# Performance work log

Measured on AMD Instinct MI355X. Metric: run time of the kernel, lower is better.

The kernel has to match this reference:

```python
import jax, jax.numpy as jnp
import numpy as np

N_VISITS, N_PROC, N_MED = 64, 32, 16
V_DIAG, V_PROC, V_MED = 2000, 1500, 4000
EMB, EMB_FF = 256, 128


def _normalize(adj):
    # row-normalize(adj + I), matching GCN.normalize
    adj = adj + np.eye(adj.shape[0], dtype=np.float32)
    rs = adj.sum(1)
    rinv = np.where(rs > 0, 1.0 / rs, 0.0).astype(np.float32)
    return (adj * rinv[:, None]).astype(np.float32)


def setup_inputs() -> dict:
    key = jax.random.key(0)
    ks = jax.random.split(key, 24)
    rng = np.random.default_rng(0)
    ehr = (rng.random((V_MED, V_MED)) < 0.01).astype(np.float32)
    ddi = (rng.random((V_MED, V_MED)) < 0.01).astype(np.float32)
    s = 0.02
    return {
        'proc_codes': jax.random.randint(ks[0], (N_VISITS, N_PROC), 0, V_DIAG + V_PROC + 2),
        'med_codes': jax.random.randint(ks[1], (N_VISITS, N_MED), 0, V_MED),
        'emb_table': jax.random.normal(ks[2], (V_DIAG + V_PROC + 2, EMB_FF)) * s,
        'conv_w': jax.random.normal(ks[3], (3,)) * 0.3,
        'conv_b': jnp.zeros((1,)),
        'wq': jax.random.normal(ks[4], (EMB_FF, EMB)) * s,
        'wk': jax.random.normal(ks[5], (EMB_FF, EMB)) * s,
        'wv': jax.random.normal(ks[6], (EMB_FF, EMB)) * s,
        'wr': jax.random.normal(ks[7], (EMB, EMB)) * s,
        'alpha': jax.random.normal(ks[8], (EMB,)),
        'beta': jax.random.normal(ks[9], (EMB,)),
        'ehr_adj_norm': jnp.asarray(_normalize(ehr)),
        'ddi_adj_norm': jnp.asarray(_normalize(ddi)),
        'ddi_adj_raw': jnp.asarray(ddi),
        'ehr_w1': jax.random.normal(ks[10], (V_MED, EMB)) * s,
        'ehr_b1': jnp.zeros((EMB,)),
        'ehr_w2': jax.random.normal(ks[11], (EMB, EMB)) * s,
        'ehr_b2': jnp.zeros((EMB,)),
        'ddi_w1': jax.random.normal(ks[12], (V_MED, EMB)) * s,
        'ddi_b1': jnp.zeros((EMB,)),
        'ddi_w2': jax.random.normal(ks[13], (EMB, EMB)) * s,
        'ddi_b2': jnp.zeros((EMB,)),
        'inter': jax.random.normal(ks[14], (1,)) * 0.1,
        'out_w1': jax.random.normal(ks[15], (3 * EMB, 2 * EMB)) * s,
        'out_b1': jnp.zeros((2 * EMB,)),
        'out_w2': jax.random.normal(ks[16], (2 * EMB, V_MED)) * s,
        'out_b2': jnp.zeros((V_MED,)),
    }


def _fastformer(x, wq, wk, wv, wr, alpha, beta):
    # x: (1, n, EMB_FF); additive linear attention (all-ones mask => no-op)
    q = x @ wq  # (1, n, EMB)
    k = x @ wk
    v = x @ wv
    scale = EMB ** -0.5
    aw = jax.nn.softmax(q * alpha * scale, axis=-1)
    gq = jnp.sum(q * aw, axis=1)              # global query (1, EMB)
    p = gq[:, None, :] * k                    # (1, n, EMB)
    bw = jax.nn.softmax(p * beta * scale, axis=-1)
    gk = jnp.sum(p * bw, axis=1)              # global key (1, EMB)
    return (gk[:, None, :] * v) @ wr + q


def _gcn(adj, w1, b1, w2, b2):
    # input x = I, so first layer support is just w1
    h = jax.nn.relu(adj @ w1 + b1)
    return adj @ (h @ w2) + b2


def reference(proc_codes, med_codes, emb_table, conv_w, conv_b, wq, wk, wv, wr, alpha, beta,
              ehr_adj_norm, ddi_adj_norm, ddi_adj_raw,
              ehr_w1, ehr_b1, ehr_w2, ehr_b2, ddi_w1, ddi_b1, ddi_w2, ddi_b2,
              inter, out_w1, out_b1, out_w2, out_b2):
    n = proc_codes.shape[0]
    # per-admission mean embedding  (n, EMB_FF)
    i2 = emb_table[proc_codes].mean(axis=1)
    # Conv1d(1,1,k=3,same) over the feature dim, then ReLU
    xp = jnp.pad(i2, ((0, 0), (1, 1)))
    i2 = jax.nn.relu(conv_w[0] * xp[:, :-2] + conv_w[1] * xp[:, 1:-1] + conv_w[2] * xp[:, 2:] + conv_b)
    feat = _fastformer(i2[None], wq, wk, wv, wr, alpha, beta)[0]  # (n, EMB)
    query = feat[-1:]
    drug_memory = _gcn(ehr_adj_norm, ehr_w1, ehr_b1, ehr_w2, ehr_b2) \
        - _gcn(ddi_adj_norm, ddi_w1, ddi_b1, ddi_w2, ddi_b2) * inter[0]
    key_w1 = jax.nn.softmax(query @ drug_memory.T, axis=-1)   # (1, V_MED)
    fact1 = key_w1 @ drug_memory                              # (1, EMB)
    # history (len(input) > 1): multi-hot med history values
    history_keys = feat[:-1]
    hv = jnp.zeros((n - 1, V_MED), dtype=feat.dtype)
    hv = hv.at[jnp.arange(n - 1)[:, None], med_codes[:-1]].set(1.0)
    visit_w = jax.nn.softmax(query @ history_keys.T, axis=-1)
    fact2 = (visit_w @ hv) @ drug_memory
    h = jnp.concatenate([query, fact1, fact2], axis=-1)       # (1, 3*EMB)
    result = jax.nn.relu(h @ out_w1 + out_b1) @ out_w2 + out_b2
    sp = jax.nn.sigmoid(result)[0]
    batch_neg = 0.0005 * jnp.einsum('i,ij,j->', sp, ddi_adj_raw, sp)
    return result, batch_neg
```

## Files before the change

kernel.cpp:

```cpp
#include <hip/hip_runtime.h>
#include <hip/hip_bf16.h>

#define NV 64
#define NP 32
#define NM 16
#define VMED 4000
#define EMB 256
#define EMBFF 128
#define CAP 128


__device__ __forceinline__ float block_sum_256(float v, float* red) {
    int t = threadIdx.x;
    red[t] = v; __syncthreads();
    for (int s = 128; s > 0; s >>= 1) { if (t < s) red[t] += red[t + s]; __syncthreads(); }
    float r = red[0]; __syncthreads();
    return r;
}
__device__ __forceinline__ float block_max_256(float v, float* red) {
    int t = threadIdx.x;
    red[t] = v; __syncthreads();
    for (int s = 128; s > 0; s >>= 1) { if (t < s) red[t] = fmaxf(red[t], red[t + s]); __syncthreads(); }
    float r = red[0]; __syncthreads();
    return r;
}

__global__ void k_embed_conv(const int* __restrict__ proc, const float* __restrict__ emb,
                             const float* __restrict__ cw, const float* __restrict__ cb,
                             float* __restrict__ i2) {
    __shared__ float sm[EMBFF + 2];
    int v = blockIdx.x, f = threadIdx.x;
    float s = 0.f;
    for (int c = 0; c < NP; c++) s += emb[proc[v * NP + c] * EMBFF + f];
    sm[f + 1] = s * (1.0f / NP);
    if (f == 0) { sm[0] = 0.f; sm[EMBFF + 1] = 0.f; }
    __syncthreads();
    float o = cw[0] * sm[f] + cw[1] * sm[f + 1] + cw[2] * sm[f + 2] + cb[0];
    i2[v * EMBFF + f] = o > 0.f ? o : 0.f;
}

__global__ void k_qkv(const float* __restrict__ i2, const float* __restrict__ wq,
                      const float* __restrict__ wk, const float* __restrict__ wv,
                      const float* __restrict__ alpha,
                      float* __restrict__ q, float* __restrict__ k, float* __restrict__ v,
                      float* __restrict__ qaw) {
    __shared__ float x[EMBFF];
    __shared__ float red[256];
    int vi = blockIdx.x, f = threadIdx.x;
    if (f < EMBFF) x[f] = i2[vi * EMBFF + f];
    __syncthreads();
    float aq = 0, ak = 0, av = 0;
    for (int e = 0; e < EMBFF; e++) {
        float xe = x[e];
        aq += xe * wq[e * EMB + f];
        ak += xe * wk[e * EMB + f];
        av += xe * wv[e * EMB + f];
    }
    q[vi * EMB + f] = aq; k[vi * EMB + f] = ak; v[vi * EMB + f] = av;
    const float scale = 0.0625f;
    float z = aq * alpha[f] * scale;
    float m = block_max_256(z, red);
    float e_ = __expf(z - m);
    float sum = block_sum_256(e_, red);
    qaw[vi * EMB + f] = aq * (e_ / sum);
}

__global__ void k_pbw(const float* __restrict__ qaw, const float* __restrict__ k,
                      const float* __restrict__ beta, float* __restrict__ pbw) {
    __shared__ float red[256];
    int vi = blockIdx.x, f = threadIdx.x;
    float g = 0;
    for (int r = 0; r < NV; r++) g += qaw[r * EMB + f];
    float p = g * k[vi * EMB + f];
    const float scale = 0.0625f;
    float z = p * beta[f] * scale;
    float m = block_max_256(z, red);
    float e_ = __expf(z - m);
    float sum = block_sum_256(e_, red);
    pbw[vi * EMB + f] = p * (e_ / sum);
}

__global__ void k_feat(const float* __restrict__ pbw, const float* __restrict__ v,
                       const float* __restrict__ q, const float* __restrict__ wr,
                       float* __restrict__ feat) {
    __shared__ float s[EMB];
    int vi = blockIdx.x, f = threadIdx.x;
    float g = 0;
    for (int r = 0; r < NV; r++) g += pbw[r * EMB + f];
    s[f] = g * v[vi * EMB + f];
    __syncthreads();
    float acc = 0;
    for (int e = 0; e < EMB; e++) acc += s[e] * wr[e * EMB + f];
    feat[vi * EMB + f] = acc + q[vi * EMB + f];
}

__global__ void k_visitw_wmed(const float* __restrict__ feat, const int* __restrict__ med,
                              float* __restrict__ w_med) {
    __shared__ float qs[EMB];
    __shared__ float vw[64];
    __shared__ float red[256];
    __shared__ float wm[VMED];
    int t = threadIdx.x;
    for (int e = t; e < EMB; e += 256) qs[e] = feat[63 * EMB + e];
    for (int i = t; i < VMED; i += 256) wm[i] = 0.f;
    __syncthreads();
    float sc = -1e30f;
    if (t < 63) {
        float a = 0;
        for (int e = 0; e < EMB; e++) a += qs[e] * feat[t * EMB + e];
        sc = a;
    }
    float m = block_max_256(sc, red);
    float e_ = (t < 63) ? __expf(sc - m) : 0.f;
    float sum = block_sum_256(e_, red);
    if (t < 63) vw[t] = e_ / sum;
    __syncthreads();
    for (int i = t; i < 63 * NM; i += 256) {
        int vv = i / NM, mm = i % NM;
        int code = med[vv * NM + mm];
        bool dup = false;
        for (int m2 = 0; m2 < mm; m2++)
            if (med[vv * NM + m2] == code) dup = true;
        if (!dup) atomicAdd(&wm[code], vw[vv]);
    }
    __syncthreads();
    for (int i = t; i < VMED; i += 256) w_med[i] = wm[i];
}

__global__ void k_spmm_relu(const float* __restrict__ adj, const float* __restrict__ w1,
                            const float* __restrict__ b1, float* __restrict__ h,
                            int* __restrict__ ccnt, int* __restrict__ cidx,
                            float* __restrict__ cval) {
    __shared__ int idx[CAP];
    __shared__ float val[CAP];
    __shared__ int cnt;
    int i = blockIdx.x, t = threadIdx.x;
    if (t == 0) cnt = 0;
    __syncthreads();
    const float4* row4 = (const float4*)(adj + (size_t)i * VMED);
    for (int j4 = t; j4 < VMED / 4; j4 += 256) {
        float4 a = row4[j4];
        if (a.x != 0.f) { int p = atomicAdd(&cnt, 1); if (p < CAP) { idx[p] = 4*j4+0; val[p] = a.x; } }
        if (a.y != 0.f) { int p = atomicAdd(&cnt, 1); if (p < CAP) { idx[p] = 4*j4+1; val[p] = a.y; } }
        if (a.z != 0.f) { int p = atomicAdd(&cnt, 1); if (p < CAP) { idx[p] = 4*j4+2; val[p] = a.z; } }
        if (a.w != 0.f) { int p = atomicAdd(&cnt, 1); if (p < CAP) { idx[p] = 4*j4+3; val[p] = a.w; } }
    }
    __syncthreads();
    int n = cnt < CAP ? cnt : CAP;
    if (t == 0) ccnt[i] = n;
    if (t < n) { cidx[i * CAP + t] = idx[t]; cval[i * CAP + t] = val[t]; }
    float acc = b1[t];
    for (int e = 0; e < n; e++) acc += val[e] * w1[idx[e] * EMB + t];
    h[(size_t)i * EMB + t] = acc > 0.f ? acc : 0.f;
}

__global__ void k_rowgemm(const float* __restrict__ h, const float* __restrict__ w2,
                          float* __restrict__ out) {
    __shared__ float x[8][EMB];
    int r0 = blockIdx.x * 8, t = threadIdx.x;
    for (int r = 0; r < 8; r++) x[r][t] = h[(size_t)(r0 + r) * EMB + t];
    __syncthreads();
    float acc[8] = {0, 0, 0, 0, 0, 0, 0, 0};
    #pragma unroll 4
    for (int e = 0; e < EMB; e++) {
        float we = w2[e * EMB + t];
        #pragma unroll
        for (int r = 0; r < 8; r++) acc[r] += x[r][e] * we;
    }
    for (int r = 0; r < 8; r++) out[(size_t)(r0 + r) * EMB + t] = acc[r];
}

__global__ void k_spmm_acc(const int* __restrict__ ccnt, const int* __restrict__ cidx,
                           const float* __restrict__ cval, const float* __restrict__ x,
                           const float* __restrict__ b2, const float* __restrict__ inter,
                           int mode, float* __restrict__ dm) {
    __shared__ int idx[CAP];
    __shared__ float val[CAP];
    int i = blockIdx.x, t = threadIdx.x;
    int n = ccnt[i];
    if (t < n) { idx[t] = cidx[i * CAP + t]; val[t] = cval[i * CAP + t]; }
    __syncthreads();
    float acc = b2[t];
    for (int e = 0; e < n; e++) acc += val[e] * x[(size_t)idx[e] * EMB + t];
    if (mode == 0) dm[(size_t)i * EMB + t] = acc;
    else           dm[(size_t)i * EMB + t] -= inter[0] * acc;
}

__global__ void k_scores(const float* __restrict__ dm, const float* __restrict__ feat,
                         float* __restrict__ s_dm) {
    __shared__ float red[256];
    int i = blockIdx.x, t = threadIdx.x;
    float s = dm[(size_t)i * EMB + t] * feat[63 * EMB + t];
    s = block_sum_256(s, red);
    if (t == 0) s_dm[i] = s;
}

__global__ void k_softmax4000(const float* __restrict__ s, float* __restrict__ out) {
    __shared__ float red[256];
    int t = threadIdx.x;
    float m = -1e30f;
    for (int i = t; i < VMED; i += 256) m = fmaxf(m, s[i]);
    m = block_max_256(m, red);
    float sum = 0;
    for (int i = t; i < VMED; i += 256) { float e = __expf(s[i] - m); out[i] = e; sum += e; }
    sum = block_sum_256(sum, red);
    float inv = 1.f / sum;
    for (int i = t; i < VMED; i += 256) out[i] *= inv;
}

__global__ void k_facts_part(const float* __restrict__ dm, const float* __restrict__ kw,
                             const float* __restrict__ wm, float* __restrict__ part1,
                             float* __restrict__ part2) {
    int f = threadIdx.x, b = blockIdx.x;
    int r0 = b * 100;
    float a1 = 0, a2 = 0;
    for (int r = r0; r < r0 + 100; r++) {
        float d = dm[(size_t)r * EMB + f];
        a1 += kw[r] * d;
        a2 += wm[r] * d;
    }
    part1[b * EMB + f] = a1;
    part2[b * EMB + f] = a2;
}

__global__ void k_hidden_part(const float* __restrict__ feat, const float* __restrict__ part1,
                              const float* __restrict__ part2, const float* __restrict__ w1,
                              float* __restrict__ hpart) {
    __shared__ float xs[16];
    int b = blockIdx.x, t = threadIdx.x;
    int e0 = b * 16;
    if (t < 16) {
        int e = e0 + t;
        float xv;
        if (e < 256) xv = feat[63 * EMB + e];
        else if (e < 512) { float s = 0; for (int p = 0; p < 40; p++) s += part1[p * EMB + (e - 256)]; xv = s; }
        else              { float s = 0; for (int p = 0; p < 40; p++) s += part2[p * EMB + (e - 512)]; xv = s; }
        xs[t] = xv;
    }
    __syncthreads();
    float a1 = 0, a2 = 0;
    #pragma unroll
    for (int i = 0; i < 16; i++) {
        int e = e0 + i;
        a1 += xs[i] * w1[e * 512 + t];
        a2 += xs[i] * w1[e * 512 + t + 256];
    }
    hpart[b * 512 + t] = a1;
    hpart[b * 512 + t + 256] = a2;
}

__global__ void k_result(const float* __restrict__ hpart, const float* __restrict__ b1,
                         const float* __restrict__ w2, const float* __restrict__ b2,
                         float* __restrict__ out, float* __restrict__ sp) {
    __shared__ float hx[512];
    __shared__ float red[8][32];
    int t = threadIdx.x;
    for (int jj = t; jj < 512; jj += 256) {
        float s = b1[jj];
        for (int p = 0; p < 48; p++) s += hpart[p * 512 + jj];
        hx[jj] = s > 0.f ? s : 0.f;
    }
    __syncthreads();
    int lane = t & 31, seg = t >> 5;
    int j = blockIdx.x * 32 + lane;
    float acc = 0;
    int e0 = seg * 64;
    #pragma unroll 8
    for (int e = e0; e < e0 + 64; e++) acc += hx[e] * w2[(size_t)e * VMED + j];
    red[seg][lane] = acc;
    __syncthreads();
    if (seg == 0) {
        float s = b2[j];
        for (int p = 0; p < 8; p++) s += red[p][lane];
        out[j] = s;
        sp[j] = 1.f / (1.f + __expf(-s));
    }
}

__global__ void k_bneg(const float* __restrict__ ddi, const float* __restrict__ sp,
                       float* __restrict__ bpart) {
    __shared__ float4 spl[VMED / 4];
    __shared__ float red[256];
    int t = threadIdx.x;
    const float4* sp4 = (const float4*)sp;
    for (int j4 = t; j4 < VMED / 4; j4 += 256) spl[j4] = sp4[j4];
    __syncthreads();
    for (int rr = 0; rr < 8; rr++) {
        int i = blockIdx.x * 8 + rr;
        const float4* row4 = (const float4*)(ddi + (size_t)i * VMED);
        float p = 0;
        for (int j4 = t; j4 < VMED / 4; j4 += 256) {
            float4 a = row4[j4];
            float4 s4 = spl[j4];
            p += a.x * s4.x + a.y * s4.y + a.z * s4.z + a.w * s4.w;
        }
        p = block_sum_256(p, red);
        if (t == 0) bpart[i] = sp[i] * p;
    }
}

__global__ void FastRx_wo_Diag_19473381720179_kernel(const float* __restrict__ bpart,
                                                     float* __restrict__ out) {
    __shared__ float red[256];
    int t = threadIdx.x;
    float s = 0;
    for (int i = t; i < VMED; i += 256) s += bpart[i];
    s = block_sum_256(s, red);
    if (t == 0) out[VMED] = 0.0005f * s;
}

extern "C" __attribute__((visibility("default")))
void kernel_launch(void* const* d_in, const int* in_sizes, int n_in,
                   void* d_out, int out_size, void* d_ws, size_t ws_size,
                   hipStream_t stream) {
    const int*   proc_codes = (const int*)d_in[0];
    const int*   med_codes  = (const int*)d_in[1];
    const float* emb_table  = (const float*)d_in[2];
    const float* conv_w     = (const float*)d_in[3];
    const float* conv_b     = (const float*)d_in[4];
    const float* wq         = (const float*)d_in[5];
    const float* wk         = (const float*)d_in[6];
    const float* wv         = (const float*)d_in[7];
    const float* wr         = (const float*)d_in[8];
    const float* alpha      = (const float*)d_in[9];
    const float* beta       = (const float*)d_in[10];
    const float* ehr_adj    = (const float*)d_in[11];
    const float* ddi_adj    = (const float*)d_in[12];
    const float* ddi_raw    = (const float*)d_in[13];
    const float* ehr_w1     = (const float*)d_in[14];
    const float* ehr_b1     = (const float*)d_in[15];
    const float* ehr_w2     = (const float*)d_in[16];
    const float* ehr_b2     = (const float*)d_in[17];
    const float* ddi_w1     = (const float*)d_in[18];
    const float* ddi_b1     = (const float*)d_in[19];
    const float* ddi_w2     = (const float*)d_in[20];
    const float* ddi_b2     = (const float*)d_in[21];
    const float* inter      = (const float*)d_in[22];
    const float* out_w1     = (const float*)d_in[23];
    const float* out_b1     = (const float*)d_in[24];
    const float* out_w2     = (const float*)d_in[25];
    const float* out_b2     = (const float*)d_in[26];
    float* out = (float*)d_out;

    float* w = (float*)d_ws;
    float* i2     = w;
    float* q      = w + 8192;
    float* k      = w + 24576;
    float* v      = w + 40960;
    float* tmpA   = w + 57344;
    float* tmpB   = w + 73728;
    float* feat   = w + 90112;
    float* wmed   = w + 106496;
    float* sdm    = w + 110592;
    float* sp     = w + 114688;
    float* bufA   = w + 118784;
    float* bufB   = bufA + 1024000;
    int*   ccnt   = (int*)(bufB + 1024000);
    int*   cidx   = ccnt + 4096;
    float* cval   = (float*)(cidx + 512000);
    float* part1  = bufA;
    float* part2  = bufA + 10240;
    float* hpart  = bufA + 20480;
    float* bpart  = bufA + 45056;

    k_embed_conv<<<NV, EMBFF, 0, stream>>>(proc_codes, emb_table, conv_w, conv_b, i2);
    k_qkv<<<NV, EMB, 0, stream>>>(i2, wq, wk, wv, alpha, q, k, v, tmpA);
    k_pbw<<<NV, EMB, 0, stream>>>(tmpA, k, beta, tmpB);
    k_feat<<<NV, EMB, 0, stream>>>(tmpB, v, q, wr, feat);
    k_visitw_wmed<<<1, 256, 0, stream>>>(feat, med_codes, wmed);

    k_spmm_relu<<<VMED, 256, 0, stream>>>(ehr_adj, ehr_w1, ehr_b1, bufA, ccnt, cidx, cval);
    k_rowgemm<<<VMED / 8, 256, 0, stream>>>(bufA, ehr_w2, bufA);
    k_spmm_acc<<<VMED, 256, 0, stream>>>(ccnt, cidx, cval, bufA, ehr_b2, inter, 0, bufB);
    k_spmm_relu<<<VMED, 256, 0, stream>>>(ddi_adj, ddi_w1, ddi_b1, bufA, ccnt, cidx, cval);
    k_rowgemm<<<VMED / 8, 256, 0, stream>>>(bufA, ddi_w2, bufA);
    k_spmm_acc<<<VMED, 256, 0, stream>>>(ccnt, cidx, cval, bufA, ddi_b2, inter, 1, bufB);

    k_scores<<<VMED, 256, 0, stream>>>(bufB, feat, sdm);
    k_softmax4000<<<1, 256, 0, stream>>>(sdm, sdm);
    k_facts_part<<<40, 256, 0, stream>>>(bufB, sdm, wmed, part1, part2);
    k_hidden_part<<<48, 256, 0, stream>>>(feat, part1, part2, out_w1, hpart);
    k_result<<<125, 256, 0, stream>>>(hpart, out_b1, out_w2, out_b2, out, sp);
    k_bneg<<<VMED / 8, 256, 0, stream>>>(ddi_raw, sp, bpart);
    FastRx_wo_Diag_19473381720179_kernel<<<1, 256, 0, stream>>>(bpart, out);
}
```

Before: 456.3 us.

## Fuse embedding/conv into QKV and merge both GCN branches into two kernels

Folds the embedding-mean and conv/ReLU step into the QKV projection kernel. It also merges the sparse first layer and dense second-layer GEMM of both GCNs into one kernel that processes 8 rows per block, with EHR and DDI handled by separate block ranges. A single combined second-layer sparse accumulation then writes drug_memory directly. This cuts kernel launches from seven to three and removes a round-trip of the intermediate hidden layer, at the cost of serial per-row sparse extraction inside each block (1000 blocks instead of 4000) and extra workspace for separate EHR and DDI index buffers.

Measured after the change: 431.1 us. -5.5%, faster.

```diff
diff --git a/kernel.cpp b/kernel.cpp
--- a/kernel.cpp
+++ b/kernel.cpp
@@ -25,44 +25,42 @@
     return r;
 }
 
-__global__ void k_embed_conv(const int* __restrict__ proc, const float* __restrict__ emb,
-                             const float* __restrict__ cw, const float* __restrict__ cb,
-                             float* __restrict__ i2) {
-    __shared__ float sm[EMBFF + 2];
-    int v = blockIdx.x, f = threadIdx.x;
-    float s = 0.f;
-    for (int c = 0; c < NP; c++) s += emb[proc[v * NP + c] * EMBFF + f];
-    sm[f + 1] = s * (1.0f / NP);
-    if (f == 0) { sm[0] = 0.f; sm[EMBFF + 1] = 0.f; }
-    __syncthreads();
-    float o = cw[0] * sm[f] + cw[1] * sm[f + 1] + cw[2] * sm[f + 2] + cb[0];
-    i2[v * EMBFF + f] = o > 0.f ? o : 0.f;
-}
-
-__global__ void k_qkv(const float* __restrict__ i2, const float* __restrict__ wq,
-                      const float* __restrict__ wk, const float* __restrict__ wv,
-                      const float* __restrict__ alpha,
+__global__ void k_ff1(const int* __restrict__ proc, const float* __restrict__ emb,
+                      const float* __restrict__ cw, const float* __restrict__ cb,
+                      const float* __restrict__ wq, const float* __restrict__ wk,
+                      const float* __restrict__ wv, const float* __restrict__ alpha,
                       float* __restrict__ q, float* __restrict__ k, float* __restrict__ v,
                       float* __restrict__ qaw) {
+    __shared__ float sm[EMBFF + 2];
     __shared__ float x[EMBFF];
     __shared__ float red[256];
-    int vi = blockIdx.x, f = threadIdx.x;
-    if (f < EMBFF) x[f] = i2[vi * EMBFF + f];
+    int vi = blockIdx.x, t = threadIdx.x;
+    if (t < EMBFF) {
+        float s = 0.f;
+        for (int c = 0; c < NP; c++) s += emb[proc[vi * NP + c] * EMBFF + t];
+        sm[t + 1] = s * (1.0f / NP);
+    }
+    if (t == 0) { sm[0] = 0.f; sm[EMBFF + 1] = 0.f; }
+    __syncthreads();
+    if (t < EMBFF) {
+        float o = cw[0] * sm[t] + cw[1] * sm[t + 1] + cw[2] * sm[t + 2] + cb[0];
+        x[t] = o > 0.f ? o : 0.f;
+    }
     __syncthreads();
     float aq = 0, ak = 0, av = 0;
     for (int e = 0; e < EMBFF; e++) {
         float xe = x[e];
-        aq += xe * wq[e * EMB + f];
-        ak += xe * wk[e * EMB + f];
-        av += xe * wv[e * EMB + f];
-    }
-    q[vi * EMB + f] = aq; k[vi * EMB + f] = ak; v[vi * EMB + f] = av;
+        aq += xe * wq[e * EMB + t];
+        ak += xe * wk[e * EMB + t];
+        av += xe * wv[e * EMB + t];
+    }
+    q[vi * EMB + t] = aq; k[vi * EMB + t] = ak; v[vi * EMB + t] = av;
     const float scale = 0.0625f;
-    float z = aq * alpha[f] * scale;
+    float z = aq * alpha[t] * scale;
     float m = block_max_256(z, red);
     float e_ = __expf(z - m);
     float sum = block_sum_256(e_, red);
-    qaw[vi * EMB + f] = aq * (e_ / sum);
+    qaw[vi * EMB + t] = aq * (e_ / sum);
 }
 
 __global__ void k_pbw(const float* __restrict__ qaw, const float* __restrict__ k,
@@ -127,63 +125,82 @@
     for (int i = t; i < VMED; i += 256) w_med[i] = wm[i];
 }
 
-__global__ void k_spmm_relu(const float* __restrict__ adj, const float* __restrict__ w1,
-                            const float* __restrict__ b1, float* __restrict__ h,
-                            int* __restrict__ ccnt, int* __restrict__ cidx,
-                            float* __restrict__ cval) {
+__global__ void k_gcn(const float* __restrict__ eadj, const float* __restrict__ dadj,
+                      const float* __restrict__ ew1, const float* __restrict__ eb1,
+                      const float* __restrict__ ew2,
+                      const float* __restrict__ dw1, const float* __restrict__ db1,
+                      const float* __restrict__ dw2,
+                      float* __restrict__ outE, float* __restrict__ outD,
+                      int* __restrict__ ccntE, int* __restrict__ cidxE, float* __restrict__ cvalE,
+                      int* __restrict__ ccntD, int* __restrict__ cidxD, float* __restrict__ cvalD) {
+    __shared__ float x[8][EMB];
     __shared__ int idx[CAP];
     __shared__ float val[CAP];
     __shared__ int cnt;
-    int i = blockIdx.x, t = threadIdx.x;
-    if (t == 0) cnt = 0;
-    __syncthreads();
-    const float4* row4 = (const float4*)(adj + (size_t)i * VMED);
-    for (int j4 = t; j4 < VMED / 4; j4 += 256) {
-        float4 a = row4[j4];
-        if (a.x != 0.f) { int p = atomicAdd(&cnt, 1); if (p < CAP) { idx[p] = 4*j4+0; val[p] = a.x; } }
-        if (a.y != 0.f) { int p = atomicAdd(&cnt, 1); if (p < CAP) { idx[p] = 4*j4+1; val[p] = a.y; } }
-        if (a.z != 0.f) { int p = atomicAdd(&cnt, 1); if (p < CAP) { idx[p] = 4*j4+2; val[p] = a.z; } }
-        if (a.w != 0.f) { int p = atomicAdd(&cnt, 1); if (p < CAP) { idx[p] = 4*j4+3; val[p] = a.w; } }
-    }
-    __syncthreads();
-    int n = cnt < CAP ? cnt : CAP;
-    if (t == 0) ccnt[i] = n;
-    if (t < n) { cidx[i * CAP + t] = idx[t]; cval[i * CAP + t] = val[t]; }
-    float acc = b1[t];
-    for (int e = 0; e < n; e++) acc += val[e] * w1[idx[e] * EMB + t];
-    h[(size_t)i * EMB + t] = acc > 0.f ? acc : 0.f;
-}
-
-__global__ void k_rowgemm(const float* __restrict__ h, const float* __restrict__ w2,
-                          float* __restrict__ out) {
-    __shared__ float x[8][EMB];
-    int r0 = blockIdx.x * 8, t = threadIdx.x;
-    for (int r = 0; r < 8; r++) x[r][t] = h[(size_t)(r0 + r) * EMB + t];
-    __syncthreads();
-    float acc[8] = {0, 0, 0, 0, 0, 0, 0, 0};
+    int b = blockIdx.x, t = threadIdx.x;
+    bool isD = b >= 500;
+    const float* adj = isD ? dadj : eadj;
+    const float* w1  = isD ? dw1  : ew1;
+    const float* b1  = isD ? db1  : eb1;
+    const float* w2  = isD ? dw2  : ew2;
+    float* outp = isD ? outD : outE;
+    int*   ccnt = isD ? ccntD : ccntE;
+    int*   cidx = isD ? cidxD : cidxE;
+    float* cval = isD ? cvalD : cvalE;
+    int r0 = (isD ? b - 500 : b) * 8;
+    for (int r = 0; r < 8; r++) {
+        int i = r0 + r;
+        if (t == 0) cnt = 0;
+        __syncthreads();
+        const float4* row4 = (const float4*)(adj + (size_t)i * VMED);
+        for (int j4 = t; j4 < VMED / 4; j4 += 256) {
+            float4 a = row4[j4];
+            if (a.x != 0.f) { int p = atomicAdd(&cnt, 1); if (p < CAP) { idx[p] = 4*j4+0; val[p] = a.x; } }
+            if (a.y != 0.f) { int p = atomicAdd(&cnt, 1); if (p < CAP) { idx[p] = 4*j4+1; val[p] = a.y; } }
+            if (a.z != 0.f) { int p = atomicAdd(&cnt, 1); if (p < CAP) { idx[p] = 4*j4+2; val[p] = a.z; } }
+            if (a.w != 0.f) { int p = atomicAdd(&cnt, 1); if (p < CAP) { idx[p] = 4*j4+3; val[p] = a.w; } }
+        }
+        __syncthreads();
+        int n = cnt < CAP ? cnt : CAP;
+        if (t == 0) ccnt[i] = n;
+        if (t < n) { cidx[i * CAP + t] = idx[t]; cval[i * CAP + t] = val[t]; }
+        float acc = b1[t];
+        for (int e = 0; e < n; e++) acc += val[e] * w1[idx[e] * EMB + t];
+        x[r][t] = acc > 0.f ? acc : 0.f;
+        __syncthreads();
+    }
+    float a[8] = {0, 0, 0, 0, 0, 0, 0, 0};
     #pragma unroll 4
     for (int e = 0; e < EMB; e++) {
         float we = w2[e * EMB + t];
         #pragma unroll
-        for (int r = 0; r < 8; r++) acc[r] += x[r][e] * we;
-    }
-    for (int r = 0; r < 8; r++) out[(size_t)(r0 + r) * EMB + t] = acc[r];
-}
-
-__global__ void k_spmm_acc(const int* __restrict__ ccnt, const int* __restrict__ cidx,
-                           const float* __restrict__ cval, const float* __restrict__ x,
-                           const float* __restrict__ b2, const float* __restrict__ inter,
-                           int mode, float* __restrict__ dm) {
+        for (int r = 0; r < 8; r++) a[r] += x[r][e] * we;
+    }
+    for (int r = 0; r < 8; r++) outp[(size_t)(r0 + r) * EMB + t] = a[r];
+}
+
+__global__ void k_acc(const int* __restrict__ ccntE, const int* __restrict__ cidxE,
+                      const float* __restrict__ cvalE,
+                      const int* __restrict__ ccntD, const int* __restrict__ cidxD,
+                      const float* __restrict__ cvalD,
+                      const float* __restrict__ xe, const float* __restrict__ xd,
+                      const float* __restrict__ b2e, const float* __restrict__ b2d,
+                      const float* __restrict__ inter, float* __restrict__ dm) {
     __shared__ int idx[CAP];
     __shared__ float val[CAP];
     int i = blockIdx.x, t = threadIdx.x;
-    int n = ccnt[i];
-    if (t < n) { idx[t] = cidx[i * CAP + t]; val[t] = cval[i * CAP + t]; }
-    __syncthreads();
-    float acc = b2[t];
-    for (int e = 0; e < n; e++) acc += val[e] * x[(size_t)idx[e] * EMB + t];
-    if (mode == 0) dm[(size_t)i * EMB + t] = acc;
-    else           dm[(size_t)i * EMB + t] -= inter[0] * acc;
+    int nE = ccntE[i];
+    if (t < nE) { idx[t] = cidxE[i * CAP + t]; val[t] = cvalE[i * CAP + t]; }
+    __syncthreads();
+    float aE = b2e[t];
+    for (int e = 0; e < nE; e++) aE += val[e] * xe[(size_t)idx[e] * EMB + t];
+    __syncthreads();
+    int nD = ccntD[i];
+    if (t < nD) { idx[t] = cidxD[i * CAP + t]; val[t] = cvalD[i * CAP + t]; }
+    __syncthreads();
+    float aD = b2d[t];
+    for (int e = 0; e < nD; e++) aD += val[e] * xd[(size_t)idx[e] * EMB + t];
+    dm[(size_t)i * EMB + t] = aE - inter[0] * aD;
 }
 
 __global__ void k_scores(const float* __restrict__ dm, const float* __restrict__ feat,
@@ -343,38 +360,42 @@
     float* out = (float*)d_out;
 
     float* w = (float*)d_ws;
-    float* i2     = w;
-    float* q      = w + 8192;
-    float* k      = w + 24576;
-    float* v      = w + 40960;
-    float* tmpA   = w + 57344;
-    float* tmpB   = w + 73728;
-    float* feat   = w + 90112;
-    float* wmed   = w + 106496;
-    float* sdm    = w + 110592;
-    float* sp     = w + 114688;
-    float* bufA   = w + 118784;
-    float* bufB   = bufA + 1024000;
-    int*   ccnt   = (int*)(bufB + 1024000);
-    int*   cidx   = ccnt + 4096;
-    float* cval   = (float*)(cidx + 512000);
+    float* q      = w;
+    float* k      = w + 16384;
+    float* v      = w + 32768;
+    float* tmpA   = w + 49152;
+    float* tmpB   = w + 65536;
+    float* feat   = w + 81920;
+    float* wmed   = w + 98304;
+    float* sdm    = w + 102400;
+    float* sp     = w + 106496;
+    float* bufA   = w + 110592;
+    float* bufC   = bufA + 1024000;
+    float* bufB   = bufC + 1024000;
+    int*   ccntE  = (int*)(bufB + 1024000);
+    int*   cidxE  = ccntE + 4096;
+    float* cvalE  = (float*)(cidxE + 512000);
+    int*   ccntD  = (int*)(cvalE + 512000);
+    int*   cidxD  = ccntD + 4096;
+    float* cvalD  = (float*)(cidxD + 512000);
     float* part1  = bufA;
     float* part2  = bufA + 10240;
     float* hpart  = bufA + 20480;
     float* bpart  = bufA + 45056;
 
-    k_embed_conv<<<NV, EMBFF, 0, stream>>>(proc_codes, emb_table, conv_w, conv_b, i2);
-    k_qkv<<<NV, EMB, 0, stream>>>(i2, wq, wk, wv, alpha, q, k, v, tmpA);
+    k_ff1<<<NV, EMB, 0, stream>>>(proc_codes, emb_table, conv_w, conv_b,
+                                  wq, wk, wv, alpha, q, k, v, tmpA);
     k_pbw<<<NV, EMB, 0, stream>>>(tmpA, k, beta, tmpB);
     k_feat<<<NV, EMB, 0, stream>>>(tmpB, v, q, wr, feat);
     k_visitw_wmed<<<1, 256, 0, stream>>>(feat, med_codes, wmed);
 
-    k_spmm_relu<<<VMED, 256, 0, stream>>>(ehr_adj, ehr_w1, ehr_b1, bufA, ccnt, cidx, cval);
-    k_rowgemm<<<VMED / 8, 256, 0, stream>>>(bufA, ehr_w2, bufA);
-    k_spmm_acc<<<VMED, 256, 0, stream>>>(ccnt, cidx, cval, bufA, ehr_b2, inter, 0, bufB);
-    k_spmm_relu<<<VMED, 256, 0, stream>>>(ddi_adj, ddi_w1, ddi_b1, bufA, ccnt, cidx, cval);
-    k_rowgemm<<<VMED / 8, 256, 0, stream>>>(bufA, ddi_w2, bufA);
-    k_spmm_acc<<<VMED, 256, 0, stream>>>(ccnt, cidx, cval, bufA, ddi_b2, inter, 1, bufB);
+    k_gcn<<<1000, 256, 0, stream>>>(ehr_adj, ddi_adj,
+                                    ehr_w1, ehr_b1, ehr_w2,
+                                    ddi_w1, ddi_b1, ddi_w2,
+                                    bufA, bufC,
+                                    ccntE, cidxE, cvalE, ccntD, cidxD, cvalD);
+    k_acc<<<VMED, 256, 0, stream>>>(ccntE, cidxE, cvalE, ccntD, cidxD, cvalD,
+                                    bufA, bufC, ehr_b2, ddi_b2, inter, bufB);
 
     k_scores<<<VMED, 256, 0, stream>>>(bufB, feat, sdm);
     k_softmax4000<<<1, 256, 0, stream>>>(sdm, sdm);
```
